# Performance work log

Measured on AMD Instinct MI355X. Metric: run time of the kernel, lower is better.

The kernel has to match this reference:

```python
import jax, jax.numpy as jnp
import numpy as np

N_HEAD = 12
LN_EPS = 1e-5


def setup_inputs() -> dict:
    key = jax.random.key(0)
    ks = jax.random.split(key, 4)
    B, T, C = 4, 2048, 768
    s = C ** -0.5
    return {
        "x": jax.random.normal(ks[0], (B, T, C), jnp.float32),
        "w_attn": jax.random.normal(ks[1], (C, 3 * C), jnp.float32) * s,
        "b_attn": jnp.zeros((3 * C,), jnp.float32),
        "w_proj": jax.random.normal(ks[2], (C, C), jnp.float32) * s,
        "b_proj": jnp.zeros((C,), jnp.float32),
        "ln1_g": jnp.ones((C,), jnp.float32),
        "ln1_b": jnp.zeros((C,), jnp.float32),
        "ln2_g": jnp.ones((C,), jnp.float32),
        "ln2_b": jnp.zeros((C,), jnp.float32),
    }


def _layernorm(x, g, b):
    mu = jnp.mean(x, axis=-1, keepdims=True)
    var = jnp.mean(jnp.square(x - mu), axis=-1, keepdims=True)
    return (x - mu) * jax.lax.rsqrt(var + LN_EPS) * g + b


def _attn(h, w_attn, b_attn, w_proj, b_proj):
    B, T, C = h.shape
    hd = C // N_HEAD
    # Faithful to torch: view(B,T,H,3*hd) then split 3*hd -> q,k,v per head
    qkv = (h @ w_attn + b_attn).reshape(B, T, N_HEAD, 3, hd)
    q = jnp.transpose(qkv[:, :, :, 0, :], (0, 2, 1, 3))  # (B,H,T,hd)
    k = jnp.transpose(qkv[:, :, :, 1, :], (0, 2, 1, 3))
    v = jnp.transpose(qkv[:, :, :, 2, :], (0, 2, 1, 3))
    # NOTE: scale is C**-0.5 (full embed dim) and there is NO causal mask,
    # exactly as in the source.
    scores = jnp.einsum("bhtd,bhsd->bhts", q, k) * (C ** -0.5)
    a = jax.nn.softmax(scores, axis=-1)
    y = jnp.einsum("bhts,bhsd->bhtd", a, v)
    y = jnp.transpose(y, (0, 2, 1, 3)).reshape(B, T, C)
    return y @ w_proj + b_proj


def reference(x, w_attn, b_attn, w_proj, b_proj, ln1_g, ln1_b, ln2_g, ln2_b):
    # Faithful to source Block.forward: attn applied twice, MLP never called.
    x = x + _attn(_layernorm(x, ln1_g, ln1_b), w_attn, b_attn, w_proj, b_proj)
    x = x + _attn(_layernorm(x, ln2_g, ln2_b), w_attn, b_attn, w_proj, b_proj)
    return x
```

## Files before the change

kernel.cpp:

```cpp
#include <hip/hip_runtime.h>


using bf16x8 = __attribute__((ext_vector_type(8))) short;
using f32x4  = __attribute__((ext_vector_type(4))) float;

__device__ __forceinline__ unsigned short f2b(float f) {
  unsigned u = __builtin_bit_cast(unsigned, f);
  u += 0x7FFFu + ((u >> 16) & 1u);
  return (unsigned short)(u >> 16);
}
__device__ __forceinline__ unsigned pk2(float a, float b) {
  unsigned ua = __builtin_bit_cast(unsigned, a);
  ua += 0x7FFFu + ((ua >> 16) & 1u);
  unsigned ub = __builtin_bit_cast(unsigned, b);
  ub += 0x7FFFu + ((ub >> 16) & 1u);
  return (ua >> 16) | (ub & 0xFFFF0000u);
}
__device__ __forceinline__ unsigned pk2t(float a, float b) {
  return (__builtin_bit_cast(unsigned, a) >> 16) |
         (__builtin_bit_cast(unsigned, b) & 0xFFFF0000u);
}

#define ASYNC16(g, l)                                                        \
  __builtin_amdgcn_global_load_lds(                                          \
      (const __attribute__((address_space(1))) void*)(g),                    \
      (__attribute__((address_space(3))) void*)(l), 16, 0, 0)

__global__ __launch_bounds__(256) void wt_kernel(const float* __restrict__ w,
                                                 unsigned short* __restrict__ wt,
                                                 int N) {
  __shared__ float tile[32][33];
  const int n0 = blockIdx.x * 32, k0 = blockIdx.y * 32;
  const int tx = threadIdx.x, ty = threadIdx.y;
#pragma unroll
  for (int i = 0; i < 32; i += 8)
    tile[ty + i][tx] = w[(size_t)(k0 + ty + i) * N + n0 + tx];
  __syncthreads();
#pragma unroll
  for (int i = 0; i < 32; i += 8)
    wt[(size_t)(n0 + ty + i) * 768 + k0 + tx] = f2b(tile[tx][ty + i]);
}

__global__ __launch_bounds__(256) void ln_kernel(const float* __restrict__ x,
                                                 const float* __restrict__ g,
                                                 const float* __restrict__ b,
                                                 unsigned short* __restrict__ h) {
  __shared__ float red[8];
  const int row = blockIdx.x;
  const int tid = threadIdx.x;
  const float* xr = x + (size_t)row * 768;
  float v0 = xr[tid], v1 = xr[tid + 256], v2 = xr[tid + 512];
  float s = v0 + v1 + v2;
  float s2 = v0 * v0 + v1 * v1 + v2 * v2;
#pragma unroll
  for (int off = 1; off < 64; off <<= 1) {
    s += __shfl_xor(s, off);
    s2 += __shfl_xor(s2, off);
  }
  if ((tid & 63) == 0) { red[tid >> 6] = s; red[4 + (tid >> 6)] = s2; }
  __syncthreads();
  const float S  = red[0] + red[1] + red[2] + red[3];
  const float S2 = red[4] + red[5] + red[6] + red[7];
  const float mu  = S * (1.0f / 768.0f);
  const float var = S2 * (1.0f / 768.0f) - mu * mu;
  const float inv = rsqrtf(var + 1e-5f);
  unsigned short* hr = h + (size_t)row * 768;
  hr[tid]       = f2b((v0 - mu) * inv * g[tid] + b[tid]);
  hr[tid + 256] = f2b((v1 - mu) * inv * g[tid + 256] + b[tid + 256]);
  hr[tid + 512] = f2b((v2 - mu) * inv * g[tid + 512] + b[tid + 512]);
}

template <int EPI>
__global__ __launch_bounds__(256, 2) void gemm_kernel(
    const unsigned short* __restrict__ A, const unsigned short* __restrict__ Bt,
    const float* __restrict__ bias, const float* __restrict__ resid,
    unsigned short* __restrict__ q, unsigned short* __restrict__ k,
    unsigned short* __restrict__ vt, float* __restrict__ outF) {
  __shared__ alignas(16) unsigned short As[128 * 32];
  __shared__ alignas(16) unsigned short Bs[128 * 32];

  const int tid = threadIdx.x;
  const int wv = tid >> 6;
  const int lane = tid & 63;
  const int quad = lane >> 4;
  const int l15 = lane & 15;
  const int m0 = blockIdx.y * 128;
  const int n0 = blockIdx.x * 128;

  const int o0 = wv * 1024 + lane * 16;
  const int rT0 = o0 >> 6, c0 = (o0 & 63) >> 1;
  const int o1 = o0 + 4096;
  const int rT1 = o1 >> 6, c1 = (o1 & 63) >> 1;

  const unsigned short* gA0 = A + (size_t)(m0 + rT0) * 768 + c0;
  const unsigned short* gA1 = A + (size_t)(m0 + rT1) * 768 + c1;
  const unsigned short* gB0 = Bt + (size_t)(n0 + rT0) * 768 + c0;
  const unsigned short* gB1 = Bt + (size_t)(n0 + rT1) * 768 + c1;
  unsigned short* lA0 = &As[wv * 512];
  unsigned short* lA1 = &As[wv * 512 + 2048];
  unsigned short* lB0 = &Bs[wv * 512];
  unsigned short* lB1 = &Bs[wv * 512 + 2048];

  f32x4 acc[4][4];
#pragma unroll
  for (int i = 0; i < 4; ++i)
#pragma unroll
    for (int j = 0; j < 4; ++j) acc[i][j] = {0.f, 0.f, 0.f, 0.f};

  const int mBase = (wv >> 1) * 64;
  const int nBase = (wv & 1) * 64;

  for (int kk = 0; kk < 24; ++kk) {
    const int ko = kk * 32;
    ASYNC16(gA0 + ko, lA0);
    ASYNC16(gA1 + ko, lA1);
    ASYNC16(gB0 + ko, lB0);
    ASYNC16(gB1 + ko, lB1);
    __syncthreads();
    bf16x8 af[4], bfv[4];
#pragma unroll
    for (int mt = 0; mt < 4; ++mt)
      af[mt] = *(const bf16x8*)&As[(mBase + mt * 16 + l15) * 32 + quad * 8];
#pragma unroll
    for (int nt = 0; nt < 4; ++nt)
      bfv[nt] = *(const bf16x8*)&Bs[(nBase + nt * 16 + l15) * 32 + quad * 8];
#pragma unroll
    for (int mt = 0; mt < 4; ++mt)
#pragma unroll
      for (int nt = 0; nt < 4; ++nt)
        acc[mt][nt] = __builtin_amdgcn_mfma_f32_16x16x32_bf16(af[mt], bfv[nt],
                                                              acc[mt][nt], 0, 0, 0);
    __syncthreads();
  }

  if constexpr (EPI == 0) {
    const float c2 = 0.052062786090587f;
#pragma unroll
    for (int mt = 0; mt < 4; ++mt) {
#pragma unroll
      for (int nt = 0; nt < 4; ++nt) {
        const int n = n0 + nBase + nt * 16 + l15;
        const int head = n / 192;
        const int rem = n - head * 192;
        const int sel = rem >> 6;
        const int d = rem & 63;
        const float bv = bias[n];
        const int mr = m0 + mBase + mt * 16 + quad * 4;
        const int bb = mr >> 11;
        const int t = mr & 2047;
        if (sel == 2) {
          const unsigned long long pk =
              (unsigned long long)pk2(acc[mt][nt][0] + bv, acc[mt][nt][1] + bv) |
              ((unsigned long long)pk2(acc[mt][nt][2] + bv, acc[mt][nt][3] + bv) << 32);
          *(unsigned long long*)&vt[(((size_t)bb * 12 + head) * 64 + d) * 2048 + t] = pk;
        } else {
          unsigned short* tgt = (sel == 0) ? q : k;
          const float sc = (sel == 0) ? c2 : 1.0f;
#pragma unroll
          for (int r = 0; r < 4; ++r)
            tgt[(((size_t)bb * 12 + head) * 2048 + t + r) * 64 + d] =
                f2b((acc[mt][nt][r] + bv) * sc);
        }
      }
    }
  } else {
#pragma unroll
    for (int mt = 0; mt < 4; ++mt) {
#pragma unroll
      for (int nt = 0; nt < 4; ++nt) {
        const int n = n0 + nBase + nt * 16 + l15;
        const float bv = bias[n];
#pragma unroll
        for (int r = 0; r < 4; ++r) {
          const int m = m0 + mBase + mt * 16 + quad * 4 + r;
          const size_t idx = (size_t)m * 768 + n;
          outF[idx] = resid[idx] + bv + acc[mt][nt][r];
        }
      }
    }
  }
}

#define PAD 68
__global__ __launch_bounds__(256, 3) void attn_kernel(
    const unsigned short* __restrict__ Q, const unsigned short* __restrict__ Km,
    const unsigned short* __restrict__ Vt, unsigned short* __restrict__ Y) {
  __shared__ alignas(16) unsigned short Ks[2][64 * PAD];
  __shared__ alignas(16) unsigned short Vs[2][64 * PAD];
  __shared__ alignas(16) unsigned short Ps[4][32 * PAD];

  const int bh = blockIdx.x;
  const int qt = blockIdx.y;
  const int tid = threadIdx.x;
  const int wv = tid >> 6;
  const int lane = tid & 63;
  const int quad = lane >> 4;
  const int l15 = lane & 15;
  const size_t bhT = (size_t)bh * 2048;

  bf16x8 qf[2][2];
#pragma unroll
  for (int g = 0; g < 2; ++g) {
    const unsigned short* qb = Q + (bhT + qt * 128 + wv * 32 + g * 16 + l15) * 64;
    qf[g][0] = *(const bf16x8*)(qb + quad * 8);
    qf[g][1] = *(const bf16x8*)(qb + 32 + quad * 8);
  }

  f32x4 o[4][2], ol[2];
#pragma unroll
  for (int dt = 0; dt < 4; ++dt)
#pragma unroll
    for (int g = 0; g < 2; ++g) o[dt][g] = {0.f, 0.f, 0.f, 0.f};
  ol[0] = {0.f, 0.f, 0.f, 0.f};
  ol[1] = {0.f, 0.f, 0.f, 0.f};
  const bf16x8 ones = {0x3F80, 0x3F80, 0x3F80, 0x3F80,
                       0x3F80, 0x3F80, 0x3F80, 0x3F80};

  const int kr = tid >> 3;
  const int kc = (tid & 7) * 8;
  const unsigned short* gK = Km + (bhT + kr) * 64 + kc;
  const unsigned short* gV = Vt + ((size_t)bh * 64 + kr) * 2048 + kc;
  const int lo0 = kr * PAD + kc;
  const int lo1 = (kr + 32) * PAD + kc;

  bf16x8 sk0 = *(const bf16x8*)(gK);
  bf16x8 sk1 = *(const bf16x8*)(gK + 32 * 64);
  bf16x8 sv0 = *(const bf16x8*)(gV);
  bf16x8 sv1 = *(const bf16x8*)(gV + 32 * 2048);

  for (int c = 0; c < 32; ++c) {
    const int p = c & 1;
    *(bf16x8*)&Ks[p][lo0] = sk0;
    *(bf16x8*)&Ks[p][lo1] = sk1;
    *(bf16x8*)&Vs[p][lo0] = sv0;
    *(bf16x8*)&Vs[p][lo1] = sv1;
    __syncthreads();
    if (c < 31) {
      sk0 = *(const bf16x8*)(gK + (size_t)(c + 1) * 4096);
      sk1 = *(const bf16x8*)(gK + (size_t)(c + 1) * 4096 + 2048);
      sv0 = *(const bf16x8*)(gV + (c + 1) * 64);
      sv1 = *(const bf16x8*)(gV + (c + 1) * 64 + 32 * 2048);
    }

    f32x4 s[2][4];
#pragma unroll
    for (int tt = 0; tt < 4; ++tt) {
      bf16x8 kf0 = *(const bf16x8*)&Ks[p][(tt * 16 + l15) * PAD + quad * 8];
      bf16x8 kf1 = *(const bf16x8*)&Ks[p][(tt * 16 + l15) * PAD + 32 + quad * 8];
      s[0][tt] = {0.f, 0.f, 0.f, 0.f};
      s[1][tt] = {0.f, 0.f, 0.f, 0.f};
      s[0][tt] = __builtin_amdgcn_mfma_f32_16x16x32_bf16(kf0, qf[0][0], s[0][tt], 0, 0, 0);
      s[1][tt] = __builtin_amdgcn_mfma_f32_16x16x32_bf16(kf0, qf[1][0], s[1][tt], 0, 0, 0);
      s[0][tt] = __builtin_amdgcn_mfma_f32_16x16x32_bf16(kf1, qf[0][1], s[0][tt], 0, 0, 0);
      s[1][tt] = __builtin_amdgcn_mfma_f32_16x16x32_bf16(kf1, qf[1][1], s[1][tt], 0, 0, 0);
    }

#pragma unroll
    for (int g = 0; g < 2; ++g)
#pragma unroll
      for (int tt = 0; tt < 4; ++tt) {
        const float e0 = __builtin_amdgcn_exp2f(s[g][tt][0]);
        const float e1 = __builtin_amdgcn_exp2f(s[g][tt][1]);
        const float e2 = __builtin_amdgcn_exp2f(s[g][tt][2]);
        const float e3 = __builtin_amdgcn_exp2f(s[g][tt][3]);
        const unsigned long long pk =
            (unsigned long long)pk2t(e0, e1) |
            ((unsigned long long)pk2t(e2, e3) << 32);
        *(unsigned long long*)&Ps[wv][(g * 16 + l15) * PAD + tt * 16 + quad * 4] = pk;
      }

#pragma unroll
    for (int ks = 0; ks < 2; ++ks) {
      bf16x8 pf0 = *(const bf16x8*)&Ps[wv][(l15) * PAD + ks * 32 + quad * 8];
      bf16x8 pf1 = *(const bf16x8*)&Ps[wv][(16 + l15) * PAD + ks * 32 + quad * 8];
      ol[0] = __builtin_amdgcn_mfma_f32_16x16x32_bf16(ones, pf0, ol[0], 0, 0, 0);
      ol[1] = __builtin_amdgcn_mfma_f32_16x16x32_bf16(ones, pf1, ol[1], 0, 0, 0);
#pragma unroll
      for (int dt = 0; dt < 4; ++dt) {
        bf16x8 vf = *(const bf16x8*)&Vs[p][(dt * 16 + l15) * PAD + ks * 32 + quad * 8];
        o[dt][0] = __builtin_amdgcn_mfma_f32_16x16x32_bf16(vf, pf0, o[dt][0], 0, 0, 0);
        o[dt][1] = __builtin_amdgcn_mfma_f32_16x16x32_bf16(vf, pf1, o[dt][1], 0, 0, 0);
      }
    }
  }

  const int b = bh / 12;
  const int head = bh - b * 12;
#pragma unroll
  for (int g = 0; g < 2; ++g) {
    const float rl = 1.0f / ol[g][0];
    const int row = qt * 128 + wv * 32 + g * 16 + l15;
    unsigned short* yb = Y + ((size_t)(b * 2048 + row)) * 768 + head * 64;
#pragma unroll
    for (int dt = 0; dt < 4; ++dt) {
      const unsigned long long pk =
          (unsigned long long)pk2(o[dt][g][0] * rl, o[dt][g][1] * rl) |
          ((unsigned long long)pk2(o[dt][g][2] * rl, o[dt][g][3] * rl) << 32);
      *(unsigned long long*)(yb + dt * 16 + quad * 4) = pk;
    }
  }
}

extern "C" void kernel_launch(void* const* d_in, const int* in_sizes, int n_in,
                              void* d_out, int out_size, void* d_ws, size_t ws_size,
                              hipStream_t stream) {
  const float* x      = (const float*)d_in[0];
  const float* w_attn = (const float*)d_in[1];
  const float* b_attn = (const float*)d_in[2];
  const float* w_proj = (const float*)d_in[3];
  const float* b_proj = (const float*)d_in[4];
  const float* ln_g[2] = {(const float*)d_in[5], (const float*)d_in[7]};
  const float* ln_b[2] = {(const float*)d_in[6], (const float*)d_in[8]};
  float* out = (float*)d_out;

  unsigned short* wAt = (unsigned short*)d_ws;
  unsigned short* wPt = wAt + 2304 * 768;
  unsigned short* h   = wPt + 768 * 768;
  unsigned short* q   = h + 8192 * 768;
  unsigned short* k   = q + 48 * 2048 * 64;
  unsigned short* vt  = k + 48 * 2048 * 64;
  unsigned short* y   = vt + 48 * 2048 * 64;

  wt_kernel<<<dim3(72, 24), dim3(32, 8), 0, stream>>>(w_attn, wAt, 2304);
  wt_kernel<<<dim3(24, 24), dim3(32, 8), 0, stream>>>(w_proj, wPt, 768);

  for (int pass = 0; pass < 2; ++pass) {
    const float* xin = pass ? (const float*)out : x;
    ln_kernel<<<8192, 256, 0, stream>>>(xin, ln_g[pass], ln_b[pass], h);
    gemm_kernel<0><<<dim3(18, 64), 256, 0, stream>>>(h, wAt, b_attn, nullptr,
                                                     q, k, vt, nullptr);
    attn_kernel<<<dim3(48, 16), 256, 0, stream>>>(q, k, vt, y);
    gemm_kernel<1><<<dim3(6, 64), 256, 0, stream>>>(y, wPt, b_proj, xin,
                                                    nullptr, nullptr, nullptr, out);
  }
}
```

Baseline: 384.8 us.

## Load K/V fragments directly from global into registers, dropping LDS staging

The attention kernel no longer stages K and V tiles through shared memory with a block-wide barrier. Each wave now loads its MFMA K and V fragments straight from global memory into registers and prefetches the next chunk right after use. This removes the LDS writes, the LDS reads and the __syncthreads per chunk. In exchange, all four waves redundantly fetch the same K/V data from global/L2, the accesses are less coalesced, and register pressure rises, which may hurt occupancy.

```diff
diff --git a/kernel.cpp b/kernel.cpp
--- a/kernel.cpp
+++ b/kernel.cpp
@@ -185,8 +185,6 @@
 __global__ __launch_bounds__(256, 3) void attn_kernel(
     const unsigned short* __restrict__ Q, const unsigned short* __restrict__ Km,
     const unsigned short* __restrict__ Vt, unsigned short* __restrict__ Y) {
-  __shared__ alignas(16) unsigned short Ks[2][64 * PAD];
-  __shared__ alignas(16) unsigned short Vs[2][64 * PAD];
   __shared__ alignas(16) unsigned short Ps[4][32 * PAD];
 
   const int bh = blockIdx.x;
@@ -216,43 +214,40 @@
   const bf16x8 ones = {0x3F80, 0x3F80, 0x3F80, 0x3F80,
                        0x3F80, 0x3F80, 0x3F80, 0x3F80};
 
-  const int kr = tid >> 3;
-  const int kc = (tid & 7) * 8;
-  const unsigned short* gK = Km + (bhT + kr) * 64 + kc;
-  const unsigned short* gV = Vt + ((size_t)bh * 64 + kr) * 2048 + kc;
-  const int lo0 = kr * PAD + kc;
-  const int lo1 = (kr + 32) * PAD + kc;
-
-  bf16x8 sk0 = *(const bf16x8*)(gK);
-  bf16x8 sk1 = *(const bf16x8*)(gK + 32 * 64);
-  bf16x8 sv0 = *(const bf16x8*)(gV);
-  bf16x8 sv1 = *(const bf16x8*)(gV + 32 * 2048);
+  const unsigned short* pK = Km + (bhT + l15) * 64 + quad * 8;
+  const unsigned short* pV = Vt + ((size_t)bh * 64 + l15) * 2048 + quad * 8;
+
+  bf16x8 kf[4][2], vf[4][2];
+#pragma unroll
+  for (int tt = 0; tt < 4; ++tt) {
+    kf[tt][0] = *(const bf16x8*)(pK + tt * 1024);
+    kf[tt][1] = *(const bf16x8*)(pK + tt * 1024 + 32);
+  }
+#pragma unroll
+  for (int dt = 0; dt < 4; ++dt) {
+    vf[dt][0] = *(const bf16x8*)(pV + (size_t)dt * 32768);
+    vf[dt][1] = *(const bf16x8*)(pV + (size_t)dt * 32768 + 32);
+  }
 
   for (int c = 0; c < 32; ++c) {
-    const int p = c & 1;
-    *(bf16x8*)&Ks[p][lo0] = sk0;
-    *(bf16x8*)&Ks[p][lo1] = sk1;
-    *(bf16x8*)&Vs[p][lo0] = sv0;
-    *(bf16x8*)&Vs[p][lo1] = sv1;
-    __syncthreads();
-    if (c < 31) {
-      sk0 = *(const bf16x8*)(gK + (size_t)(c + 1) * 4096);
-      sk1 = *(const bf16x8*)(gK + (size_t)(c + 1) * 4096 + 2048);
-      sv0 = *(const bf16x8*)(gV + (c + 1) * 64);
-      sv1 = *(const bf16x8*)(gV + (c + 1) * 64 + 32 * 2048);
-    }
-
     f32x4 s[2][4];
 #pragma unroll
     for (int tt = 0; tt < 4; ++tt) {
-      bf16x8 kf0 = *(const bf16x8*)&Ks[p][(tt * 16 + l15) * PAD + quad * 8];
-      bf16x8 kf1 = *(const bf16x8*)&Ks[p][(tt * 16 + l15) * PAD + 32 + quad * 8];
       s[0][tt] = {0.f, 0.f, 0.f, 0.f};
       s[1][tt] = {0.f, 0.f, 0.f, 0.f};
-      s[0][tt] = __builtin_amdgcn_mfma_f32_16x16x32_bf16(kf0, qf[0][0], s[0][tt], 0, 0, 0);
-      s[1][tt] = __builtin_amdgcn_mfma_f32_16x16x32_bf16(kf0, qf[1][0], s[1][tt], 0, 0, 0);
-      s[0][tt] = __builtin_amdgcn_mfma_f32_16x16x32_bf16(kf1, qf[0][1], s[0][tt], 0, 0, 0);
-      s[1][tt] = __builtin_amdgcn_mfma_f32_16x16x32_bf16(kf1, qf[1][1], s[1][tt], 0, 0, 0);
+      s[0][tt] = __builtin_amdgcn_mfma_f32_16x16x32_bf16(kf[tt][0], qf[0][0], s[0][tt], 0, 0, 0);
+      s[1][tt] = __builtin_amdgcn_mfma_f32_16x16x32_bf16(kf[tt][0], qf[1][0], s[1][tt], 0, 0, 0);
+      s[0][tt] = __builtin_amdgcn_mfma_f32_16x16x32_bf16(kf[tt][1], qf[0][1], s[0][tt], 0, 0, 0);
+      s[1][tt] = __builtin_amdgcn_mfma_f32_16x16x32_bf16(kf[tt][1], qf[1][1], s[1][tt], 0, 0, 0);
+    }
+
+    if (c < 31) {
+      const unsigned short* pKn = pK + (size_t)(c + 1) * 4096;
+#pragma unroll
+      for (int tt = 0; tt < 4; ++tt) {
+        kf[tt][0] = *(const bf16x8*)(pKn + tt * 1024);
+        kf[tt][1] = *(const bf16x8*)(pKn + tt * 1024 + 32);
+      }
     }
 
 #pragma unroll
@@ -277,9 +272,17 @@
       ol[1] = __builtin_amdgcn_mfma_f32_16x16x32_bf16(ones, pf1, ol[1], 0, 0, 0);
 #pragma unroll
       for (int dt = 0; dt < 4; ++dt) {
-        bf16x8 vf = *(const bf16x8*)&Vs[p][(dt * 16 + l15) * PAD + ks * 32 + quad * 8];
-        o[dt][0] = __builtin_amdgcn_mfma_f32_16x16x32_bf16(vf, pf0, o[dt][0], 0, 0, 0);
-        o[dt][1] = __builtin_amdgcn_mfma_f32_16x16x32_bf16(vf, pf1, o[dt][1], 0, 0, 0);
+        o[dt][0] = __builtin_amdgcn_mfma_f32_16x16x32_bf16(vf[dt][ks], pf0, o[dt][0], 0, 0, 0);
+        o[dt][1] = __builtin_amdgcn_mfma_f32_16x16x32_bf16(vf[dt][ks], pf1, o[dt][1], 0, 0, 0);
+      }
+    }
+
+    if (c < 31) {
+      const unsigned short* pVn = pV + (c + 1) * 64;
+#pragma unroll
+      for (int dt = 0; dt < 4; ++dt) {
+        vf[dt][0] = *(const bf16x8*)(pVn + (size_t)dt * 32768);
+        vf[dt][1] = *(const bf16x8*)(pVn + (size_t)dt * 32768 + 32);
       }
     }
   }
```

After: 598.3 us. +55.5%, slower.

## Restructure attention inner loop with 32x32 MFMA, register P, async swizzled LDS loads

Applied to the files above, without the earlier changes.

Rewrites the attention kernel to use 32x32x16 bf16 MFMAs and to keep the softmax probabilities in registers, rearranging them with v_permlane32_swap instead of a round trip through LDS. The row sum is now accumulated in scalar registers rather than through an extra MFMA against a ones vector. K/V tiles are loaded straight into LDS with global_load_lds into XOR-swizzled, unpadded buffers, which frees LDS and drops the register staging. The aim is to cut LDS traffic, instruction count and bank conflicts, at the cost of more intricate lane layout logic and a dependence on the gfx950 permlane instruction.

```diff
diff --git a/kernel.cpp b/kernel.cpp
--- a/kernel.cpp
+++ b/kernel.cpp
@@ -3,6 +3,7 @@
 
 using bf16x8 = __attribute__((ext_vector_type(8))) short;
 using f32x4  = __attribute__((ext_vector_type(4))) float;
+using f32x16 = __attribute__((ext_vector_type(16))) float;
 
 __device__ __forceinline__ unsigned short f2b(float f) {
   unsigned u = __builtin_bit_cast(unsigned, f);
@@ -16,15 +17,20 @@
   ub += 0x7FFFu + ((ub >> 16) & 1u);
   return (ua >> 16) | (ub & 0xFFFF0000u);
 }
-__device__ __forceinline__ unsigned pk2t(float a, float b) {
-  return (__builtin_bit_cast(unsigned, a) >> 16) |
-         (__builtin_bit_cast(unsigned, b) & 0xFFFF0000u);
+
+__device__ __forceinline__ bf16x8 mk8(unsigned a, unsigned b, unsigned c,
+                                      unsigned d) {
+  union { unsigned u[4]; bf16x8 v; } x;
+  x.u[0] = a; x.u[1] = b; x.u[2] = c; x.u[3] = d;
+  return x.v;
 }
 
 #define ASYNC16(g, l)                                                        \
   __builtin_amdgcn_global_load_lds(                                          \
       (const __attribute__((address_space(1))) void*)(g),                    \
       (__attribute__((address_space(3))) void*)(l), 16, 0, 0)
+
+#define PLSWAP(a, b) asm("v_permlane32_swap_b32 %0, %1" : "+v"(a), "+v"(b))
 
 __global__ __launch_bounds__(256) void wt_kernel(const float* __restrict__ w,
                                                  unsigned short* __restrict__ wt,
@@ -181,122 +187,135 @@
   }
 }
 
-#define PAD 68
 __global__ __launch_bounds__(256, 3) void attn_kernel(
     const unsigned short* __restrict__ Q, const unsigned short* __restrict__ Km,
     const unsigned short* __restrict__ Vt, unsigned short* __restrict__ Y) {
-  __shared__ alignas(16) unsigned short Ks[2][64 * PAD];
-  __shared__ alignas(16) unsigned short Vs[2][64 * PAD];
-  __shared__ alignas(16) unsigned short Ps[4][32 * PAD];
-
-  const int bh = blockIdx.x;
-  const int qt = blockIdx.y;
-  const int tid = threadIdx.x;
-  const int wv = tid >> 6;
+  __shared__ alignas(16) unsigned short Ks[2][64 * 64];
+  __shared__ alignas(16) unsigned short Vs[2][64 * 64];
+
+  const int bh   = blockIdx.x;
+  const int qt   = blockIdx.y;
+  const int tid  = threadIdx.x;
+  const int wv   = tid >> 6;
   const int lane = tid & 63;
-  const int quad = lane >> 4;
-  const int l15 = lane & 15;
+  const int l31  = lane & 31;
+  const int hi   = lane >> 5;
+  const int s7   = l31 & 7;
   const size_t bhT = (size_t)bh * 2048;
 
-  bf16x8 qf[2][2];
-#pragma unroll
-  for (int g = 0; g < 2; ++g) {
-    const unsigned short* qb = Q + (bhT + qt * 128 + wv * 32 + g * 16 + l15) * 64;
-    qf[g][0] = *(const bf16x8*)(qb + quad * 8);
-    qf[g][1] = *(const bf16x8*)(qb + 32 + quad * 8);
-  }
-
-  f32x4 o[4][2], ol[2];
-#pragma unroll
-  for (int dt = 0; dt < 4; ++dt)
-#pragma unroll
-    for (int g = 0; g < 2; ++g) o[dt][g] = {0.f, 0.f, 0.f, 0.f};
-  ol[0] = {0.f, 0.f, 0.f, 0.f};
-  ol[1] = {0.f, 0.f, 0.f, 0.f};
-  const bf16x8 ones = {0x3F80, 0x3F80, 0x3F80, 0x3F80,
-                       0x3F80, 0x3F80, 0x3F80, 0x3F80};
-
-  const int kr = tid >> 3;
-  const int kc = (tid & 7) * 8;
-  const unsigned short* gK = Km + (bhT + kr) * 64 + kc;
-  const unsigned short* gV = Vt + ((size_t)bh * 64 + kr) * 2048 + kc;
-  const int lo0 = kr * PAD + kc;
-  const int lo1 = (kr + 32) * PAD + kc;
-
-  bf16x8 sk0 = *(const bf16x8*)(gK);
-  bf16x8 sk1 = *(const bf16x8*)(gK + 32 * 64);
-  bf16x8 sv0 = *(const bf16x8*)(gV);
-  bf16x8 sv1 = *(const bf16x8*)(gV + 32 * 2048);
+  bf16x8 qf[4];
+  {
+    const unsigned short* qb =
+        Q + (bhT + qt * 128 + wv * 32 + l31) * 64 + hi * 8;
+#pragma unroll
+    for (int ks = 0; ks < 4; ++ks) qf[ks] = *(const bf16x8*)(qb + ks * 16);
+  }
+
+  const int L0 = wv * 1024 + (lane << 4);
+  const int L1 = L0 + 4096;
+  const int r0 = L0 >> 7, b0 = (L0 & 127) ^ ((r0 & 7) << 4);
+  const int r1 = L1 >> 7, b1 = (L1 & 127) ^ ((r1 & 7) << 4);
+  const unsigned short* kg0 = Km + (bhT + r0) * 64 + (b0 >> 1);
+  const unsigned short* kg1 = Km + (bhT + r1) * 64 + (b1 >> 1);
+  const unsigned short* vg0 = Vt + ((size_t)bh * 64 + r0) * 2048 + (b0 >> 1);
+  const unsigned short* vg1 = Vt + ((size_t)bh * 64 + r1) * 2048 + (b1 >> 1);
+  const int kb0 = wv * 512, kb1 = wv * 512 + 2048;
+
+  f32x16 o0, o1;
+#pragma unroll
+  for (int i = 0; i < 16; ++i) { o0[i] = 0.f; o1[i] = 0.f; }
+  float l_acc = 0.f;
+
+  ASYNC16(kg0, &Ks[0][kb0]);
+  ASYNC16(kg1, &Ks[0][kb1]);
+  ASYNC16(vg0, &Vs[0][kb0]);
+  ASYNC16(vg1, &Vs[0][kb1]);
+  __syncthreads();
 
   for (int c = 0; c < 32; ++c) {
     const int p = c & 1;
-    *(bf16x8*)&Ks[p][lo0] = sk0;
-    *(bf16x8*)&Ks[p][lo1] = sk1;
-    *(bf16x8*)&Vs[p][lo0] = sv0;
-    *(bf16x8*)&Vs[p][lo1] = sv1;
+    if (c < 31) {
+      const int ka = (c + 1) * 4096, va = (c + 1) * 64;
+      ASYNC16(kg0 + ka, &Ks[p ^ 1][kb0]);
+      ASYNC16(kg1 + ka, &Ks[p ^ 1][kb1]);
+      ASYNC16(vg0 + va, &Vs[p ^ 1][kb0]);
+      ASYNC16(vg1 + va, &Vs[p ^ 1][kb1]);
+    }
+    const unsigned short* Kp = &Ks[p][0];
+    const unsigned short* Vp = &Vs[p][0];
+
+#pragma unroll
+    for (int tt = 0; tt < 2; ++tt) {
+      f32x16 s;
+#pragma unroll
+      for (int i = 0; i < 16; ++i) s[i] = 0.f;
+#pragma unroll
+      for (int ks = 0; ks < 4; ++ks) {
+        const int off = tt * 4096 + l31 * 128 + (((ks * 2 + hi) ^ s7) << 4);
+        bf16x8 kf = *(const bf16x8*)&Kp[off >> 1];
+        s = __builtin_amdgcn_mfma_f32_32x32x16_bf16(kf, qf[ks], s, 0, 0, 0);
+      }
+
+      unsigned dw[8];
+      float lc = 0.f;
+#pragma unroll
+      for (int r2 = 0; r2 < 8; ++r2) {
+        const float e0 = __builtin_amdgcn_exp2f(s[2 * r2]);
+        const float e1 = __builtin_amdgcn_exp2f(s[2 * r2 + 1]);
+        const unsigned u0 = __builtin_bit_cast(unsigned, e0) & 0xFFFF0000u;
+        const unsigned u1 = __builtin_bit_cast(unsigned, e1) & 0xFFFF0000u;
+        lc += __builtin_bit_cast(float, u0) + __builtin_bit_cast(float, u1);
+        dw[r2] = (u0 >> 16) | u1;
+      }
+      l_acc += lc;
+
+      PLSWAP(dw[0], dw[2]);
+      PLSWAP(dw[1], dw[3]);
+      PLSWAP(dw[4], dw[6]);
+      PLSWAP(dw[5], dw[7]);
+      const bf16x8 pf0 = mk8(dw[0], dw[1], dw[2], dw[3]);
+      const bf16x8 pf1 = mk8(dw[4], dw[5], dw[6], dw[7]);
+
+#pragma unroll
+      for (int dt = 0; dt < 2; ++dt) {
+        const int vb = dt * 4096 + l31 * 128;
+        const int kv0 = tt * 2, kv1 = tt * 2 + 1;
+        bf16x8 vf0 = *(const bf16x8*)&Vp[(vb + (((kv0 * 2 + hi) ^ s7) << 4)) >> 1];
+        bf16x8 vf1 = *(const bf16x8*)&Vp[(vb + (((kv1 * 2 + hi) ^ s7) << 4)) >> 1];
+        if (dt == 0) {
+          o0 = __builtin_amdgcn_mfma_f32_32x32x16_bf16(vf0, pf0, o0, 0, 0, 0);
+          o0 = __builtin_amdgcn_mfma_f32_32x32x16_bf16(vf1, pf1, o0, 0, 0, 0);
+        } else {
+          o1 = __builtin_amdgcn_mfma_f32_32x32x16_bf16(vf0, pf0, o1, 0, 0, 0);
+          o1 = __builtin_amdgcn_mfma_f32_32x32x16_bf16(vf1, pf1, o1, 0, 0, 0);
+        }
+      }
+    }
     __syncthreads();
-    if (c < 31) {
-      sk0 = *(const bf16x8*)(gK + (size_t)(c + 1) * 4096);
-      sk1 = *(const bf16x8*)(gK + (size_t)(c + 1) * 4096 + 2048);
-      sv0 = *(const bf16x8*)(gV + (c + 1) * 64);
-      sv1 = *(const bf16x8*)(gV + (c + 1) * 64 + 32 * 2048);
-    }
-
-    f32x4 s[2][4];
-#pragma unroll
-    for (int tt = 0; tt < 4; ++tt) {
-      bf16x8 kf0 = *(const bf16x8*)&Ks[p][(tt * 16 + l15) * PAD + quad * 8];
-      bf16x8 kf1 = *(const bf16x8*)&Ks[p][(tt * 16 + l15) * PAD + 32 + quad * 8];
-      s[0][tt] = {0.f, 0.f, 0.f, 0.f};
-      s[1][tt] = {0.f, 0.f, 0.f, 0.f};
-      s[0][tt] = __builtin_amdgcn_mfma_f32_16x16x32_bf16(kf0, qf[0][0], s[0][tt], 0, 0, 0);
-      s[1][tt] = __builtin_amdgcn_mfma_f32_16x16x32_bf16(kf0, qf[1][0], s[1][tt], 0, 0, 0);
-      s[0][tt] = __builtin_amdgcn_mfma_f32_16x16x32_bf16(kf1, qf[0][1], s[0][tt], 0, 0, 0);
-      s[1][tt] = __builtin_amdgcn_mfma_f32_16x16x32_bf16(kf1, qf[1][1], s[1][tt], 0, 0, 0);
-    }
-
-#pragma unroll
-    for (int g = 0; g < 2; ++g)
-#pragma unroll
-      for (int tt = 0; tt < 4; ++tt) {
-        const float e0 = __builtin_amdgcn_exp2f(s[g][tt][0]);
-        const float e1 = __builtin_amdgcn_exp2f(s[g][tt][1]);
-        const float e2 = __builtin_amdgcn_exp2f(s[g][tt][2]);
-        const float e3 = __builtin_amdgcn_exp2f(s[g][tt][3]);
-        const unsigned long long pk =
-            (unsigned long long)pk2t(e0, e1) |
-            ((unsigned long long)pk2t(e2, e3) << 32);
-        *(unsigned long long*)&Ps[wv][(g * 16 + l15) * PAD + tt * 16 + quad * 4] = pk;
-      }
-
-#pragma unroll
-    for (int ks = 0; ks < 2; ++ks) {
-      bf16x8 pf0 = *(const bf16x8*)&Ps[wv][(l15) * PAD + ks * 32 + quad * 8];
-      bf16x8 pf1 = *(const bf16x8*)&Ps[wv][(16 + l15) * PAD + ks * 32 + quad * 8];
-      ol[0] = __builtin_amdgcn_mfma_f32_16x16x32_bf16(ones, pf0, ol[0], 0, 0, 0);
-      ol[1] = __builtin_amdgcn_mfma_f32_16x16x32_bf16(ones, pf1, ol[1], 0, 0, 0);
-#pragma unroll
-      for (int dt = 0; dt < 4; ++dt) {
-        bf16x8 vf = *(const bf16x8*)&Vs[p][(dt * 16 + l15) * PAD + ks * 32 + quad * 8];
-        o[dt][0] = __builtin_amdgcn_mfma_f32_16x16x32_bf16(vf, pf0, o[dt][0], 0, 0, 0);
-        o[dt][1] = __builtin_amdgcn_mfma_f32_16x16x32_bf16(vf, pf1, o[dt][1], 0, 0, 0);
-      }
-    }
-  }
+  }
+
+  unsigned la = __builtin_bit_cast(unsigned, l_acc), lb = la;
+  PLSWAP(la, lb);
+  const float l_tot =
+      l_acc + __builtin_bit_cast(float, hi ? la : lb);
+  const float rl = 1.0f / l_tot;
 
   const int b = bh / 12;
   const int head = bh - b * 12;
-#pragma unroll
-  for (int g = 0; g < 2; ++g) {
-    const float rl = 1.0f / ol[g][0];
-    const int row = qt * 128 + wv * 32 + g * 16 + l15;
-    unsigned short* yb = Y + ((size_t)(b * 2048 + row)) * 768 + head * 64;
-#pragma unroll
-    for (int dt = 0; dt < 4; ++dt) {
+  const int row = qt * 128 + wv * 32 + l31;
+  unsigned short* yb = Y + ((size_t)(b * 2048 + row)) * 768 + head * 64;
+#pragma unroll
+  for (int dt = 0; dt < 2; ++dt) {
+#pragma unroll
+    for (int g4 = 0; g4 < 4; ++g4) {
+      const int d = dt * 32 + g4 * 8 + hi * 4;
+      const float a0 = (dt ? o1[g4 * 4 + 0] : o0[g4 * 4 + 0]) * rl;
+      const float a1 = (dt ? o1[g4 * 4 + 1] : o0[g4 * 4 + 1]) * rl;
+      const float a2 = (dt ? o1[g4 * 4 + 2] : o0[g4 * 4 + 2]) * rl;
+      const float a3 = (dt ? o1[g4 * 4 + 3] : o0[g4 * 4 + 3]) * rl;
       const unsigned long long pk =
-          (unsigned long long)pk2(o[dt][g][0] * rl, o[dt][g][1] * rl) |
-          ((unsigned long long)pk2(o[dt][g][2] * rl, o[dt][g][3] * rl) << 32);
-      *(unsigned long long*)(yb + dt * 16 + quad * 4) = pk;
+          (unsigned long long)pk2(a0, a1) | ((unsigned long long)pk2(a2, a3) << 32);
+      *(unsigned long long*)(yb + d) = pk;
     }
   }
 }
```

Measured after the change: 386.6 us. Within noise of the previous version (+0.5%).
